# Kernel optimization log

Hardware: AMD Instinct MI355X
Metric: run time of the kernel (lower is better)

Reference implementation:

```python
import jax, jax.numpy as jnp
import numpy as np

NUM_HEADS = 8


def _proj(W, b, x):
    # x: [B, C, N] channel-wise 1x1 conv == matmul over channels
    return jnp.einsum('oc,bcn->bon', W, x) + b[None, :, None]


def setup_inputs() -> dict:
    key = jax.random.key(0)
    ks = jax.random.split(key, 8)
    B, C, H, W = 4, 512, 24, 24
    inp = {
        'feat0': jax.random.normal(ks[0], (B, C, H, W), jnp.float32),
        'feat1': jax.random.normal(ks[1], (B, C, H, W), jnp.float32),
        'feat2': jax.random.normal(ks[2], (B, C, H, W), jnp.float32),
        'Wq': jax.random.normal(ks[3], (C, C), jnp.float32) * 0.02,
        'bq': jnp.zeros((C,), jnp.float32),
        'Wk': jax.random.normal(ks[4], (C, C), jnp.float32) * 0.02,
        'bk': jnp.zeros((C,), jnp.float32),
        'Wv': jax.random.normal(ks[5], (C, C), jnp.float32) * 0.02,
        'bv': jnp.zeros((C,), jnp.float32),
        'Wo': jax.random.normal(ks[6], (C, C), jnp.float32) * 0.02,
        'bo': jnp.zeros((C,), jnp.float32),
    }
    return inp


def reference(feat0, feat1, feat2, Wq, bq, Wk, bk, Wv, bv, Wo, bo):
    feats = [feat0, feat1, feat2]
    B, C, H, W = feat0.shape
    h = NUM_HEADS
    d = C // h
    scale = d ** -0.5

    # Precompute K/V once per feature (the torch loop redundantly recomputes them;
    # the math is identical).
    flat = [f.reshape(B, C, H * W) for f in feats]
    K = jnp.concatenate([_proj(Wk, bk, x).reshape(B, h, d, -1) for x in flat], axis=-1)  # [B,h,d,KV]
    V = jnp.concatenate([_proj(Wv, bv, x).reshape(B, h, d, -1) for x in flat], axis=-1)  # [B,h,d,KV]

    outs = []
    for feat, x in zip(feats, flat):
        q = _proj(Wq, bq, x).reshape(B, h, d, H * W)  # [B,h,d,N]
        attn = jax.nn.softmax(jnp.einsum('bhdn,bhdm->bhnm', q, K) * scale, axis=-1)
        out = jnp.einsum('bhnm,bhdm->bhdn', attn, V).reshape(B, C, H * W)
        out = _proj(Wo, bo, out).reshape(B, C, H, W)
        outs.append(feat + out)
    return tuple(outs)
```

## Files before the change

kernel.cpp:

```cpp
#include <hip/hip_runtime.h>


using bf16x8 = __attribute__((ext_vector_type(8))) short;
using f32x4  = __attribute__((ext_vector_type(4))) float;
using f32x16 = __attribute__((ext_vector_type(16))) float;
using u32x4  = __attribute__((ext_vector_type(4))) unsigned int;
using u16x4  = __attribute__((ext_vector_type(4))) unsigned short;
using u16x8  = __attribute__((ext_vector_type(8))) unsigned short;

#define MFMA16(a, b, c) __builtin_amdgcn_mfma_f32_16x16x32_bf16((a), (b), (c), 0, 0, 0)
#define MFMA32(a, b, c) __builtin_amdgcn_mfma_f32_32x32x16_bf16((a), (b), (c), 0, 0, 0)

__device__ __forceinline__ unsigned short f2bf(float f) {
  unsigned int u = __float_as_uint(f);
  return (unsigned short)((u + 0x7fffu + ((u >> 16) & 1u)) >> 16);
}

__device__ __forceinline__ f32x16 zero16() {
  f32x16 z;
#pragma unroll
  for (int i = 0; i < 16; ++i) z[i] = 0.f;
  return z;
}

__global__ __launch_bounds__(256) void k_prep(
    const float* __restrict__ Wq, const float* __restrict__ Wk,
    const float* __restrict__ Wv, const float* __restrict__ Wo,
    const float* __restrict__ f0, const float* __restrict__ f1,
    const float* __restrict__ f2,
    unsigned short* __restrict__ Wf, unsigned short* __restrict__ Xf) {
  __shared__ unsigned short tile[64][65];
  const int bid = blockIdx.x;
  const int t = threadIdx.x;
  if (bid < 1024) {
    int idx = (bid * 256 + t) * 4;
    int p   = idx >> 18;
    int rem = idx & 262143;
    int o = rem >> 9, c0 = rem & 511;
    const float* s = p == 0 ? Wq : p == 1 ? Wk : p == 2 ? Wv : Wo;
    f32x4 v = *(const f32x4*)(s + rem);
    u16x4 pk;
    pk[0] = f2bf(v[0]); pk[1] = f2bf(v[1]); pk[2] = f2bf(v[2]); pk[3] = f2bf(v[3]);
    int mt = o >> 6, fr = (o & 63) >> 4, lr = o & 15;
    int ks = c0 >> 5, lg = (c0 & 31) >> 3, j0 = c0 & 7;
    size_t off = (size_t)((((p * 8 + mt) * 16 + ks) * 4 + fr)) * 512 +
                 (lg * 16 + lr) * 8 + j0;
    *(u16x4*)(Wf + off) = pk;
    return;
  }
  const int id = bid - 1024;
  const int nt = id % 9;
  const int ct = (id / 9) % 8;
  const int z  = id / 72;
  const int b = z / 3, f = z % 3;
  const float* src = (f == 0 ? f0 : f == 1 ? f1 : f2) + b * (512 * 576);

#pragma unroll
  for (int i = 0; i < 16; ++i) {
    int idx = i * 256 + t;
    int cc = idx >> 6, nn = idx & 63;
    tile[cc][nn] = f2bf(src[(ct * 64 + cc) * 576 + nt * 64 + nn]);
  }
  __syncthreads();
  const int ntw = f * 9 + nt;
#pragma unroll
  for (int i = 0; i < 4; ++i) {
    int slot = i * 256 + t;
    int nn = slot >> 4, cq = slot & 15;
    int cl = cq * 4;
    int c  = ct * 64 + cl;
    int fc = nn >> 4, lr = nn & 15;
    int ks = c >> 5, lg = (c & 31) >> 3, j0 = c & 7;
    u16x4 pk;
    pk[0] = tile[cl][nn]; pk[1] = tile[cl + 1][nn];
    pk[2] = tile[cl + 2][nn]; pk[3] = tile[cl + 3][nn];
    size_t off = (size_t)((((b * 27 + ntw) * 16 + ks) * 4 + fc)) * 512 +
                 (lg * 16 + lr) * 8 + j0;
    *(u16x4*)(Xf + off) = pk;
  }
}

__global__ __launch_bounds__(256) void k_gemm_qkv(
    const unsigned short* __restrict__ Wf, const unsigned short* __restrict__ Xf,
    const float* __restrict__ bq, const float* __restrict__ bk,
    const float* __restrict__ bv,
    unsigned short* __restrict__ Qf, unsigned short* __restrict__ Kf,
    unsigned short* __restrict__ Vf) {
  const int id = blockIdx.x;
  const int xcd = id & 7, s = id >> 3;
  const int b = xcd >> 1, par = xcd & 1;
  const int p = s / 54, bx = (s % 54) * 2 + par;
  const int t = threadIdx.x, w = t >> 6, l = t & 63, lg = l >> 4, lr = l & 15;
  const int wid = bx * 4 + w;
  const int mt = wid / 54, rest = wid % 54;
  const int ntw = rest >> 1, half = rest & 1;
  const unsigned short* A = Wf + (size_t)(p * 8 + mt) * 16 * 2048 + l * 8;
  const unsigned short* B = Xf + (size_t)(b * 27 + ntw) * 16 * 2048 +
                            half * 1024 + l * 8;

  f32x4 acc[4][2];
#pragma unroll
  for (int fr = 0; fr < 4; ++fr)
#pragma unroll
    for (int fc = 0; fc < 2; ++fc) acc[fr][fc] = (f32x4){0.f, 0.f, 0.f, 0.f};

#pragma unroll 2
  for (int ks = 0; ks < 16; ++ks) {
    bf16x8 af[4], bfv[2];
#pragma unroll
    for (int fr = 0; fr < 4; ++fr)
      af[fr] = *(const bf16x8*)(A + ks * 2048 + fr * 512);
#pragma unroll
    for (int fc = 0; fc < 2; ++fc)
      bfv[fc] = *(const bf16x8*)(B + ks * 2048 + fc * 512);
#pragma unroll
    for (int fr = 0; fr < 4; ++fr)
#pragma unroll
      for (int fc = 0; fc < 2; ++fc)
        acc[fr][fc] = MFMA16(af[fr], bfv[fc], acc[fr][fc]);
  }

  const float* bias = p == 0 ? bq : p == 1 ? bk : bv;
  const int bh = b * 8 + mt;
  const int ck = ntw * 2 + half;
#pragma unroll
  for (int fr = 0; fr < 4; ++fr) {
    f32x4 b4 = *(const f32x4*)(bias + mt * 64 + fr * 16 + lg * 4);
#pragma unroll
    for (int fc = 0; fc < 2; ++fc) {
      if (p < 2) {
        unsigned short* outF = (p == 0) ? Qf : Kf;
        u16x4 pk;
#pragma unroll
        for (int r = 0; r < 4; ++r) {
          float v = acc[fr][fc][r] + b4[r];
          if (p == 0) v *= 0.18033688f;
          pk[r] = f2bf(v);
        }
        size_t off = ((size_t)bh * 54 + ck) * 2048 + fr * 512 +
                     ((lg >> 1) * 32 + fc * 16 + lr) * 8 + (lg & 1) * 4;
        *(u16x4*)(outF + off) = pk;
      } else {
        size_t base = ((size_t)bh * 54 + ck) * 2048 +
                      ((fr >> 1) * 2 + fc) * 512 +
                      (((lr >> 3) & 1) * 32 + (fr & 1) * 16 + lg * 4) * 8 +
                      (lr & 7);
#pragma unroll
        for (int r = 0; r < 4; ++r)
          Vf[base + r * 8] = f2bf(acc[fr][fc][r] + b4[r]);
      }
    }
  }
}

__global__ __launch_bounds__(256, 4) void k_attn(
    const unsigned short* __restrict__ Qf, const unsigned short* __restrict__ Kf,
    const unsigned short* __restrict__ Vf, unsigned short* __restrict__ Of) {
  const int id = blockIdx.x;
  const int xcd = id & 7, slot = id >> 3;
  const int bh = xcd * 4 + (slot / 54);
  const int qt = slot % 54;
  const int b = bh >> 3, h = bh & 7;
  const int t = threadIdx.x, w = t >> 6, l = t & 63;
  const int lr = l & 31, hi = l >> 5;

  __shared__ float Obuf[4][32][68];
  __shared__ float Lbuf[4][32];

  const unsigned short* Qb = Qf + ((size_t)bh * 54 + qt) * 2048 + l * 8;
  bf16x8 bq[4];
#pragma unroll
  for (int kf = 0; kf < 4; ++kf) bq[kf] = *(const bf16x8*)(Qb + kf * 512);

  f32x16 oacc[2];
  oacc[0] = zero16(); oacc[1] = zero16();
  float ls = 0.f;

  const unsigned short* Kb = Kf + (size_t)bh * 54 * 2048 + l * 8;
  const unsigned short* Vb = Vf + (size_t)bh * 54 * 2048 + l * 8;

#pragma unroll 1
  for (int ck = w; ck < 54; ck += 4) {
    const unsigned short* kc = Kb + ck * 2048;
    const unsigned short* vc = Vb + ck * 2048;
    bf16x8 ak[4];
#pragma unroll
    for (int i = 0; i < 4; ++i) ak[i] = *(const bf16x8*)(kc + i * 512);

    f32x16 sA = zero16();
#pragma unroll
    for (int kf = 0; kf < 4; ++kf) sA = MFMA32(ak[kf], bq[kf], sA);

    bf16x8 vb[4];
#pragma unroll
    for (int i = 0; i < 4; ++i) vb[i] = *(const bf16x8*)(vc + i * 512);

    unsigned int W[8];
    float a0 = 0.f, a1 = 0.f;
#pragma unroll
    for (int u = 0; u < 8; ++u) {
      float e0, e1;
      asm("v_exp_f32 %0, %1" : "=v"(e0) : "v"(sA[2 * u]));
      asm("v_exp_f32 %0, %1" : "=v"(e1) : "v"(sA[2 * u + 1]));
      a0 += e0; a1 += e1;
      asm("v_cvt_pk_bf16_f32 %0, %1, %2" : "=v"(W[u]) : "v"(e0), "v"(e1));
    }
    ls += a0 + a1;

    unsigned int fw[2][4];
#pragma unroll
    for (int kf = 0; kf < 2; ++kf)
#pragma unroll
      for (int wd = 0; wd < 2; ++wd) {
        unsigned int lo  = W[4 * kf + wd];
        unsigned int hw  = W[4 * kf + 2 + wd];
        unsigned int pub = hi ? lo : hw;
        unsigned int rcv = (unsigned int)__shfl_xor((int)pub, 32, 64);
        fw[kf][wd]     = hi ? rcv : lo;
        fw[kf][2 + wd] = hi ? hw : rcv;
      }
    u32x4 w0, w1;
    w0[0] = fw[0][0]; w0[1] = fw[0][1]; w0[2] = fw[0][2]; w0[3] = fw[0][3];
    w1[0] = fw[1][0]; w1[1] = fw[1][1]; w1[2] = fw[1][2]; w1[3] = fw[1][3];
    bf16x8 pa0 = __builtin_bit_cast(bf16x8, w0);
    bf16x8 pa1 = __builtin_bit_cast(bf16x8, w1);

    oacc[0] = MFMA32(pa0, vb[0], oacc[0]);
    oacc[0] = MFMA32(pa1, vb[1], oacc[0]);
    oacc[1] = MFMA32(pa0, vb[2], oacc[1]);
    oacc[1] = MFMA32(pa1, vb[3], oacc[1]);
  }

  float lt = ls + __shfl_xor(ls, 32, 64);
  if (l < 32) Lbuf[w][lr] = lt;
#pragma unroll
  for (int dt = 0; dt < 2; ++dt)
#pragma unroll
    for (int r = 0; r < 16; ++r)
      Obuf[w][(r & 3) + 8 * (r >> 2) + 4 * hi][dt * 32 + lr] = oacc[dt][r];
  __syncthreads();

  const int n = t >> 3, d0 = (t & 7) * 8;
  float ltot = Lbuf[0][n] + Lbuf[1][n] + Lbuf[2][n] + Lbuf[3][n];
  float linv = 1.0f / ltot;
  u16x8 o8;
#pragma unroll
  for (int i = 0; i < 8; ++i) {
    float ov = Obuf[0][n][d0 + i] + Obuf[1][n][d0 + i] +
               Obuf[2][n][d0 + i] + Obuf[3][n][d0 + i];
    o8[i] = f2bf(ov * linv);
  }
  size_t off = (size_t)((((b * 27 + (qt >> 1)) * 16 + h * 2 + (d0 >> 5)) * 4 +
                         (qt & 1) * 2 + (n >> 4))) * 512 +
               ((d0 >> 3) & 3) * 128 + (n & 15) * 8;
  *(u16x8*)(Of + off) = o8;
}

__global__ __launch_bounds__(256) void k_gemm_out(
    const unsigned short* __restrict__ Wf, const unsigned short* __restrict__ Of,
    const float* __restrict__ bo,
    const float* __restrict__ f0, const float* __restrict__ f1,
    const float* __restrict__ f2, float* __restrict__ out) {
  const int z = blockIdx.z, b = z / 3, f = z % 3;
  const int t = threadIdx.x, w = t >> 6, l = t & 63, lg = l >> 4, lr = l & 15;
  const int wid = blockIdx.x * 4 + w;
  const int mt = wid / 18, rest = wid % 18;
  const int ntw = rest >> 1, half = rest & 1;
  const int o0 = mt * 64;
  const unsigned short* A = Wf + (size_t)(3 * 8 + mt) * 16 * 2048 + l * 8;
  const unsigned short* B = Of + (size_t)(b * 27 + f * 9 + ntw) * 16 * 2048 +
                            half * 1024 + l * 8;

  f32x4 acc[4][2];
#pragma unroll
  for (int fr = 0; fr < 4; ++fr)
#pragma unroll
    for (int fc = 0; fc < 2; ++fc) acc[fr][fc] = (f32x4){0.f, 0.f, 0.f, 0.f};

#pragma unroll 2
  for (int ks = 0; ks < 16; ++ks) {
    bf16x8 af[4], bfv[2];
#pragma unroll
    for (int fr = 0; fr < 4; ++fr)
      af[fr] = *(const bf16x8*)(A + ks * 2048 + fr * 512);
#pragma unroll
    for (int fc = 0; fc < 2; ++fc)
      bfv[fc] = *(const bf16x8*)(B + ks * 2048 + fc * 512);
#pragma unroll
    for (int fr = 0; fr < 4; ++fr)
#pragma unroll
      for (int fc = 0; fc < 2; ++fc)
        acc[fr][fc] = MFMA16(af[fr], bfv[fc], acc[fr][fc]);
  }

  const float* ft = f == 0 ? f0 : f == 1 ? f1 : f2;
#pragma unroll
  for (int fr = 0; fr < 4; ++fr) {
    f32x4 b4 = *(const f32x4*)(bo + o0 + fr * 16 + lg * 4);
#pragma unroll
    for (int fc = 0; fc < 2; ++fc) {
      int ncol = ntw * 64 + half * 32 + fc * 16 + lr;
#pragma unroll
      for (int r = 0; r < 4; ++r) {
        int o = o0 + fr * 16 + lg * 4 + r;
        out[((f * 4 + b) * 512 + o) * 576 + ncol] =
            acc[fr][fc][r] + b4[r] + ft[(b * 512 + o) * 576 + ncol];
      }
    }
  }
}

extern "C" void kernel_launch(void* const* d_in, const int* in_sizes, int n_in,
                              void* d_out, int out_size, void* d_ws, size_t ws_size,
                              hipStream_t stream) {
  const float* f0 = (const float*)d_in[0];
  const float* f1 = (const float*)d_in[1];
  const float* f2 = (const float*)d_in[2];
  const float* Wq = (const float*)d_in[3];
  const float* bq = (const float*)d_in[4];
  const float* Wk = (const float*)d_in[5];
  const float* bk = (const float*)d_in[6];
  const float* Wv = (const float*)d_in[7];
  const float* bv = (const float*)d_in[8];
  const float* Wo = (const float*)d_in[9];
  const float* bo = (const float*)d_in[10];
  float* out = (float*)d_out;

  char* ws = (char*)d_ws;
  unsigned short* Wf = (unsigned short*)(ws);
  unsigned short* Xf = (unsigned short*)(ws + 2097152);
  unsigned short* Qf = (unsigned short*)(ws + 9175040);
  unsigned short* Kf = (unsigned short*)(ws + 16252928);
  unsigned short* Vf = (unsigned short*)(ws + 23330816);
  unsigned short* Of = Xf;

  k_prep<<<dim3(1888), 256, 0, stream>>>(Wq, Wk, Wv, Wo, f0, f1, f2, Wf, Xf);
  k_gemm_qkv<<<dim3(1296), 256, 0, stream>>>(Wf, Xf, bq, bk, bv, Qf, Kf, Vf);
  k_attn<<<dim3(1728), 256, 0, stream>>>(Qf, Kf, Vf, Of);
  k_gemm_out<<<dim3(36, 1, 12), 256, 0, stream>>>(Wf, Of, bo, f0, f1, f2, out);
}
```

Measured before the change: 90.00 us.

## Process two query tiles per attention block to reuse K/V fragment loads

Each attention block now handles two 32-row query tiles instead of one, so every K and V chunk loaded from global memory feeds both tiles' score and PV MFMAs. The grid is halved to 864 blocks and the launch bounds drop to 3 waves per SIMD to make room for the doubled accumulators. The goal is to halve K/V global/L2 traffic and amortize load latency across more MFMA work. The trade-off is higher register pressure, lower occupancy, fewer blocks for load balance, and an extra LDS reduction pass with additional barriers in the epilogue.

```diff
diff --git a/kernel.cpp b/kernel.cpp
--- a/kernel.cpp
+++ b/kernel.cpp
@@ -153,28 +153,66 @@
   }
 }
 
-__global__ __launch_bounds__(256, 4) void k_attn(
+__device__ __forceinline__ void softmax_pa(const f32x16& s, float& lsum,
+                                           bf16x8& pa0, bf16x8& pa1, int hi) {
+  unsigned int W[8];
+  float a0 = 0.f, a1 = 0.f;
+#pragma unroll
+  for (int u = 0; u < 8; ++u) {
+    float e0, e1;
+    asm("v_exp_f32 %0, %1" : "=v"(e0) : "v"(s[2 * u]));
+    asm("v_exp_f32 %0, %1" : "=v"(e1) : "v"(s[2 * u + 1]));
+    a0 += e0; a1 += e1;
+    asm("v_cvt_pk_bf16_f32 %0, %1, %2" : "=v"(W[u]) : "v"(e0), "v"(e1));
+  }
+  lsum += a0 + a1;
+  unsigned int fw[2][4];
+#pragma unroll
+  for (int kf = 0; kf < 2; ++kf)
+#pragma unroll
+    for (int wd = 0; wd < 2; ++wd) {
+      unsigned int lo  = W[4 * kf + wd];
+      unsigned int hw  = W[4 * kf + 2 + wd];
+      unsigned int pub = hi ? lo : hw;
+      unsigned int rcv = (unsigned int)__shfl_xor((int)pub, 32, 64);
+      fw[kf][wd]     = hi ? rcv : lo;
+      fw[kf][2 + wd] = hi ? hw : rcv;
+    }
+  u32x4 w0, w1;
+  w0[0] = fw[0][0]; w0[1] = fw[0][1]; w0[2] = fw[0][2]; w0[3] = fw[0][3];
+  w1[0] = fw[1][0]; w1[1] = fw[1][1]; w1[2] = fw[1][2]; w1[3] = fw[1][3];
+  pa0 = __builtin_bit_cast(bf16x8, w0);
+  pa1 = __builtin_bit_cast(bf16x8, w1);
+}
+
+__global__ __launch_bounds__(256, 3) void k_attn(
     const unsigned short* __restrict__ Qf, const unsigned short* __restrict__ Kf,
     const unsigned short* __restrict__ Vf, unsigned short* __restrict__ Of) {
   const int id = blockIdx.x;
   const int xcd = id & 7, slot = id >> 3;
-  const int bh = xcd * 4 + (slot / 54);
-  const int qt = slot % 54;
+  const int bh = xcd * 4 + (slot / 27);
+  const int g  = slot % 27;
   const int b = bh >> 3, h = bh & 7;
   const int t = threadIdx.x, w = t >> 6, l = t & 63;
   const int lr = l & 31, hi = l >> 5;
+  const int t0 = g * 2, t1 = g * 2 + 1;
 
   __shared__ float Obuf[4][32][68];
-  __shared__ float Lbuf[4][32];
-
-  const unsigned short* Qb = Qf + ((size_t)bh * 54 + qt) * 2048 + l * 8;
-  bf16x8 bq[4];
-#pragma unroll
-  for (int kf = 0; kf < 4; ++kf) bq[kf] = *(const bf16x8*)(Qb + kf * 512);
-
-  f32x16 oacc[2];
-  oacc[0] = zero16(); oacc[1] = zero16();
-  float ls = 0.f;
+  __shared__ float Lbuf[4][2][32];
+
+  const unsigned short* Qb0 = Qf + ((size_t)bh * 54 + t0) * 2048 + l * 8;
+  const unsigned short* Qb1 = Qf + ((size_t)bh * 54 + t1) * 2048 + l * 8;
+  bf16x8 bq0[4], bq1[4];
+#pragma unroll
+  for (int kf = 0; kf < 4; ++kf) {
+    bq0[kf] = *(const bf16x8*)(Qb0 + kf * 512);
+    bq1[kf] = *(const bf16x8*)(Qb1 + kf * 512);
+  }
+
+  f32x16 o0acc[2], o1acc[2];
+  o0acc[0] = zero16(); o0acc[1] = zero16();
+  o1acc[0] = zero16(); o1acc[1] = zero16();
+  float ls0 = 0.f, ls1 = 0.f;
 
   const unsigned short* Kb = Kf + (size_t)bh * 54 * 2048 + l * 8;
   const unsigned short* Vb = Vf + (size_t)bh * 54 * 2048 + l * 8;
@@ -183,77 +221,80 @@
   for (int ck = w; ck < 54; ck += 4) {
     const unsigned short* kc = Kb + ck * 2048;
     const unsigned short* vc = Vb + ck * 2048;
-    bf16x8 ak[4];
+    bf16x8 ak[4], vb[4];
 #pragma unroll
     for (int i = 0; i < 4; ++i) ak[i] = *(const bf16x8*)(kc + i * 512);
-
-    f32x16 sA = zero16();
-#pragma unroll
-    for (int kf = 0; kf < 4; ++kf) sA = MFMA32(ak[kf], bq[kf], sA);
-
-    bf16x8 vb[4];
 #pragma unroll
     for (int i = 0; i < 4; ++i) vb[i] = *(const bf16x8*)(vc + i * 512);
 
-    unsigned int W[8];
-    float a0 = 0.f, a1 = 0.f;
-#pragma unroll
-    for (int u = 0; u < 8; ++u) {
-      float e0, e1;
-      asm("v_exp_f32 %0, %1" : "=v"(e0) : "v"(sA[2 * u]));
-      asm("v_exp_f32 %0, %1" : "=v"(e1) : "v"(sA[2 * u + 1]));
-      a0 += e0; a1 += e1;
-      asm("v_cvt_pk_bf16_f32 %0, %1, %2" : "=v"(W[u]) : "v"(e0), "v"(e1));
-    }
-    ls += a0 + a1;
-
-    unsigned int fw[2][4];
-#pragma unroll
-    for (int kf = 0; kf < 2; ++kf)
-#pragma unroll
-      for (int wd = 0; wd < 2; ++wd) {
-        unsigned int lo  = W[4 * kf + wd];
-        unsigned int hw  = W[4 * kf + 2 + wd];
-        unsigned int pub = hi ? lo : hw;
-        unsigned int rcv = (unsigned int)__shfl_xor((int)pub, 32, 64);
-        fw[kf][wd]     = hi ? rcv : lo;
-        fw[kf][2 + wd] = hi ? hw : rcv;
-      }
-    u32x4 w0, w1;
-    w0[0] = fw[0][0]; w0[1] = fw[0][1]; w0[2] = fw[0][2]; w0[3] = fw[0][3];
-    w1[0] = fw[1][0]; w1[1] = fw[1][1]; w1[2] = fw[1][2]; w1[3] = fw[1][3];
-    bf16x8 pa0 = __builtin_bit_cast(bf16x8, w0);
-    bf16x8 pa1 = __builtin_bit_cast(bf16x8, w1);
-
-    oacc[0] = MFMA32(pa0, vb[0], oacc[0]);
-    oacc[0] = MFMA32(pa1, vb[1], oacc[0]);
-    oacc[1] = MFMA32(pa0, vb[2], oacc[1]);
-    oacc[1] = MFMA32(pa1, vb[3], oacc[1]);
-  }
-
-  float lt = ls + __shfl_xor(ls, 32, 64);
-  if (l < 32) Lbuf[w][lr] = lt;
+    f32x16 s0 = zero16();
+#pragma unroll
+    for (int kf = 0; kf < 4; ++kf) s0 = MFMA32(ak[kf], bq0[kf], s0);
+    bf16x8 pa0, pa1;
+    softmax_pa(s0, ls0, pa0, pa1, hi);
+    o0acc[0] = MFMA32(pa0, vb[0], o0acc[0]);
+    o0acc[0] = MFMA32(pa1, vb[1], o0acc[0]);
+    o0acc[1] = MFMA32(pa0, vb[2], o0acc[1]);
+    o0acc[1] = MFMA32(pa1, vb[3], o0acc[1]);
+
+    f32x16 s1 = zero16();
+#pragma unroll
+    for (int kf = 0; kf < 4; ++kf) s1 = MFMA32(ak[kf], bq1[kf], s1);
+    softmax_pa(s1, ls1, pa0, pa1, hi);
+    o1acc[0] = MFMA32(pa0, vb[0], o1acc[0]);
+    o1acc[0] = MFMA32(pa1, vb[1], o1acc[0]);
+    o1acc[1] = MFMA32(pa0, vb[2], o1acc[1]);
+    o1acc[1] = MFMA32(pa1, vb[3], o1acc[1]);
+  }
+
+  float lt0 = ls0 + __shfl_xor(ls0, 32, 64);
+  float lt1 = ls1 + __shfl_xor(ls1, 32, 64);
+  if (l < 32) { Lbuf[w][0][lr] = lt0; Lbuf[w][1][lr] = lt1; }
 #pragma unroll
   for (int dt = 0; dt < 2; ++dt)
 #pragma unroll
     for (int r = 0; r < 16; ++r)
-      Obuf[w][(r & 3) + 8 * (r >> 2) + 4 * hi][dt * 32 + lr] = oacc[dt][r];
+      Obuf[w][(r & 3) + 8 * (r >> 2) + 4 * hi][dt * 32 + lr] = o0acc[dt][r];
   __syncthreads();
 
   const int n = t >> 3, d0 = (t & 7) * 8;
-  float ltot = Lbuf[0][n] + Lbuf[1][n] + Lbuf[2][n] + Lbuf[3][n];
-  float linv = 1.0f / ltot;
-  u16x8 o8;
-#pragma unroll
-  for (int i = 0; i < 8; ++i) {
-    float ov = Obuf[0][n][d0 + i] + Obuf[1][n][d0 + i] +
-               Obuf[2][n][d0 + i] + Obuf[3][n][d0 + i];
-    o8[i] = f2bf(ov * linv);
-  }
-  size_t off = (size_t)((((b * 27 + (qt >> 1)) * 16 + h * 2 + (d0 >> 5)) * 4 +
-                         (qt & 1) * 2 + (n >> 4))) * 512 +
-               ((d0 >> 3) & 3) * 128 + (n & 15) * 8;
-  *(u16x8*)(Of + off) = o8;
+  {
+    float lt = Lbuf[0][0][n] + Lbuf[1][0][n] + Lbuf[2][0][n] + Lbuf[3][0][n];
+    float linv = 1.0f / lt;
+    u16x8 o8;
+#pragma unroll
+    for (int i = 0; i < 8; ++i) {
+      float ov = Obuf[0][n][d0 + i] + Obuf[1][n][d0 + i] +
+                 Obuf[2][n][d0 + i] + Obuf[3][n][d0 + i];
+      o8[i] = f2bf(ov * linv);
+    }
+    size_t off = (size_t)((((b * 27 + (t0 >> 1)) * 16 + h * 2 + (d0 >> 5)) * 4 +
+                           (t0 & 1) * 2 + (n >> 4))) * 512 +
+                 ((d0 >> 3) & 3) * 128 + (n & 15) * 8;
+    *(u16x8*)(Of + off) = o8;
+  }
+  __syncthreads();
+#pragma unroll
+  for (int dt = 0; dt < 2; ++dt)
+#pragma unroll
+    for (int r = 0; r < 16; ++r)
+      Obuf[w][(r & 3) + 8 * (r >> 2) + 4 * hi][dt * 32 + lr] = o1acc[dt][r];
+  __syncthreads();
+  {
+    float lt = Lbuf[0][1][n] + Lbuf[1][1][n] + Lbuf[2][1][n] + Lbuf[3][1][n];
+    float linv = 1.0f / lt;
+    u16x8 o8;
+#pragma unroll
+    for (int i = 0; i < 8; ++i) {
+      float ov = Obuf[0][n][d0 + i] + Obuf[1][n][d0 + i] +
+                 Obuf[2][n][d0 + i] + Obuf[3][n][d0 + i];
+      o8[i] = f2bf(ov * linv);
+    }
+    size_t off = (size_t)((((b * 27 + (t1 >> 1)) * 16 + h * 2 + (d0 >> 5)) * 4 +
+                           (t1 & 1) * 2 + (n >> 4))) * 512 +
+                 ((d0 >> 3) & 3) * 128 + (n & 15) * 8;
+    *(u16x8*)(Of + off) = o8;
+  }
 }
 
 __global__ __launch_bounds__(256) void k_gemm_out(
@@ -336,6 +377,6 @@
 
   k_prep<<<dim3(1888), 256, 0, stream>>>(Wq, Wk, Wv, Wo, f0, f1, f2, Wf, Xf);
   k_gemm_qkv<<<dim3(1296), 256, 0, stream>>>(Wf, Xf, bq, bk, bv, Qf, Kf, Vf);
-  k_attn<<<dim3(1728), 256, 0, stream>>>(Qf, Kf, Vf, Of);
+  k_attn<<<dim3(864), 256, 0, stream>>>(Qf, Kf, Vf, Of);
   k_gemm_out<<<dim3(36, 1, 12), 256, 0, stream>>>(Wf, Of, bo, f0, f1, f2, out);
 }
```

Result: slower. 96.39 us (+7.1%).

## Share double-buffered K/V tiles in LDS across two query tiles per block

Applied to the files above, without the earlier changes.

Restructures the attention kernel so each block has two waves, each owning its own query tile and sweeping all 54 KV chunks. This replaces the old scheme of four waves splitting the KV range for a single query tile. K and V chunks are staged into LDS with direct global-to-LDS loads and double buffered, so each KV tile fetched from global memory serves two query tiles. The cross-wave partial-sum reduction is removed, since each wave normalizes and writes its own output. In exchange there are far fewer waves in flight, each wave runs a longer serial loop, and every iteration needs a block barrier, whose ordering with the asynchronous LDS loads is not explicitly waited on.

```diff
diff --git a/kernel.cpp b/kernel.cpp
--- a/kernel.cpp
+++ b/kernel.cpp
@@ -21,6 +21,12 @@
 #pragma unroll
   for (int i = 0; i < 16; ++i) z[i] = 0.f;
   return z;
+}
+
+__device__ __forceinline__ void gload_lds16(const void* g, void* l) {
+  __builtin_amdgcn_global_load_lds(
+      (const __attribute__((address_space(1))) void*)g,
+      (__attribute__((address_space(3))) void*)l, 16, 0, 0);
 }
 
 __global__ __launch_bounds__(256) void k_prep(
@@ -153,19 +159,21 @@
   }
 }
 
-__global__ __launch_bounds__(256, 4) void k_attn(
+__global__ __launch_bounds__(128, 4) void k_attn(
     const unsigned short* __restrict__ Qf, const unsigned short* __restrict__ Kf,
     const unsigned short* __restrict__ Vf, unsigned short* __restrict__ Of) {
   const int id = blockIdx.x;
   const int xcd = id & 7, slot = id >> 3;
-  const int bh = xcd * 4 + (slot / 54);
-  const int qt = slot % 54;
+  const int bh = xcd * 4 + (slot / 27);
+  const int g  = slot % 27;
   const int b = bh >> 3, h = bh & 7;
   const int t = threadIdx.x, w = t >> 6, l = t & 63;
   const int lr = l & 31, hi = l >> 5;
-
-  __shared__ float Obuf[4][32][68];
-  __shared__ float Lbuf[4][32];
+  const int qt = g * 2 + w;
+
+  __shared__ unsigned short kv[2][4096];
+  __shared__ float Obuf[2][32][68];
+  __shared__ float Lbuf[2][32];
 
   const unsigned short* Qb = Qf + ((size_t)bh * 54 + qt) * 2048 + l * 8;
   bf16x8 bq[4];
@@ -176,16 +184,29 @@
   oacc[0] = zero16(); oacc[1] = zero16();
   float ls = 0.f;
 
-  const unsigned short* Kb = Kf + (size_t)bh * 54 * 2048 + l * 8;
-  const unsigned short* Vb = Vf + (size_t)bh * 54 * 2048 + l * 8;
-
+  const unsigned short* gsrc =
+      (w == 0 ? Kf : Vf) + (size_t)bh * 54 * 2048 + l * 8;
+
+#pragma unroll
+  for (int s2 = 0; s2 < 4; ++s2)
+    gload_lds16(gsrc + s2 * 512, (char*)&kv[0][w * 2048] + s2 * 1024);
+
+  int cur = 0;
 #pragma unroll 1
-  for (int ck = w; ck < 54; ck += 4) {
-    const unsigned short* kc = Kb + ck * 2048;
-    const unsigned short* vc = Vb + ck * 2048;
+  for (int ck = 0; ck < 54; ++ck) {
+    __syncthreads();
+    if (ck + 1 < 54) {
+      const unsigned short* gs = gsrc + (size_t)(ck + 1) * 2048;
+#pragma unroll
+      for (int s2 = 0; s2 < 4; ++s2)
+        gload_lds16(gs + s2 * 512, (char*)&kv[cur ^ 1][w * 2048] + s2 * 1024);
+    }
+
+    const unsigned short* kc = &kv[cur][0];
+    const unsigned short* vc = &kv[cur][2048];
     bf16x8 ak[4];
 #pragma unroll
-    for (int i = 0; i < 4; ++i) ak[i] = *(const bf16x8*)(kc + i * 512);
+    for (int i = 0; i < 4; ++i) ak[i] = *(const bf16x8*)(kc + i * 512 + l * 8);
 
     f32x16 sA = zero16();
 #pragma unroll
@@ -193,7 +214,7 @@
 
     bf16x8 vb[4];
 #pragma unroll
-    for (int i = 0; i < 4; ++i) vb[i] = *(const bf16x8*)(vc + i * 512);
+    for (int i = 0; i < 4; ++i) vb[i] = *(const bf16x8*)(vc + i * 512 + l * 8);
 
     unsigned int W[8];
     float a0 = 0.f, a1 = 0.f;
@@ -229,6 +250,8 @@
     oacc[0] = MFMA32(pa1, vb[1], oacc[0]);
     oacc[1] = MFMA32(pa0, vb[2], oacc[1]);
     oacc[1] = MFMA32(pa1, vb[3], oacc[1]);
+
+    cur ^= 1;
   }
 
   float lt = ls + __shfl_xor(ls, 32, 64);
@@ -238,22 +261,20 @@
 #pragma unroll
     for (int r = 0; r < 16; ++r)
       Obuf[w][(r & 3) + 8 * (r >> 2) + 4 * hi][dt * 32 + lr] = oacc[dt][r];
-  __syncthreads();
-
-  const int n = t >> 3, d0 = (t & 7) * 8;
-  float ltot = Lbuf[0][n] + Lbuf[1][n] + Lbuf[2][n] + Lbuf[3][n];
-  float linv = 1.0f / ltot;
-  u16x8 o8;
-#pragma unroll
-  for (int i = 0; i < 8; ++i) {
-    float ov = Obuf[0][n][d0 + i] + Obuf[1][n][d0 + i] +
-               Obuf[2][n][d0 + i] + Obuf[3][n][d0 + i];
-    o8[i] = f2bf(ov * linv);
-  }
-  size_t off = (size_t)((((b * 27 + (qt >> 1)) * 16 + h * 2 + (d0 >> 5)) * 4 +
-                         (qt & 1) * 2 + (n >> 4))) * 512 +
-               ((d0 >> 3) & 3) * 128 + (n & 15) * 8;
-  *(u16x8*)(Of + off) = o8;
+
+  const int n = l >> 1, dh = l & 1;
+  float linv = 1.0f / Lbuf[w][n];
+#pragma unroll
+  for (int part = 0; part < 4; ++part) {
+    const int d0 = dh * 32 + part * 8;
+    u16x8 o8;
+#pragma unroll
+    for (int i = 0; i < 8; ++i) o8[i] = f2bf(Obuf[w][n][d0 + i] * linv);
+    size_t off = (size_t)((((b * 27 + (qt >> 1)) * 16 + h * 2 + (d0 >> 5)) * 4 +
+                           (qt & 1) * 2 + (n >> 4))) * 512 +
+                 ((d0 >> 3) & 3) * 128 + (n & 15) * 8;
+    *(u16x8*)(Of + off) = o8;
+  }
 }
 
 __global__ __launch_bounds__(256) void k_gemm_out(
@@ -336,6 +357,6 @@
 
   k_prep<<<dim3(1888), 256, 0, stream>>>(Wq, Wk, Wv, Wo, f0, f1, f2, Wf, Xf);
   k_gemm_qkv<<<dim3(1296), 256, 0, stream>>>(Wf, Xf, bq, bk, bv, Qf, Kf, Vf);
-  k_attn<<<dim3(1728), 256, 0, stream>>>(Qf, Kf, Vf, Of);
+  k_attn<<<dim3(864), 128, 0, stream>>>(Qf, Kf, Vf, Of);
   k_gemm_out<<<dim3(36, 1, 12), 256, 0, stream>>>(Wf, Of, bo, f0, f1, f2, out);
 }
```

Result: slower. 103.7 us (+15.3%).
